# Kernel optimization log

Hardware: AMD Instinct MI355X
Metric: run time of the kernel (lower is better)

## Reference

```python
import jax, jax.numpy as jnp
import numpy as np
from jax import lax

BSZ, BEAM, VOCAB, D = 32, 4, 50257, 1024
MAXLEN = 64
L = MAXLEN + 2            # tokens buffer length (bos + maxlen+1 slots)
SLEN = MAXLEN + 1         # scores buffer length
PAD, EOS, UNK = 1, 2, 3
TEMP = 1.0
LEN_PEN = 1.0
UNK_PEN = 0.0
NEG = jnp.float32(-1e9)   # stand-in for -inf (safe for grads)


def setup_inputs() -> dict:
    key = jax.random.key(0)
    k1, k2, k3 = jax.random.split(key, 3)
    # 0.02 scaling keeps logits in a realistic range
    emb = jax.random.normal(k1, (VOCAB, D), jnp.float32) * 0.02
    W_out = jax.random.normal(k2, (D, VOCAB), jnp.float32) * 0.02
    pos_emb = jax.random.normal(k3, (SLEN, D), jnp.float32) * 0.02
    return {"emb": emb, "W_out": W_out, "pos_emb": pos_emb}


def _decode(emb, W_out, pos_emb, tokens, step):
    # stand-in decoder: prev-token embedding + pos embedding -> vocab logits
    prev = lax.dynamic_index_in_dim(tokens, step, axis=1, keepdims=False)  # [bbsz]
    h = emb[prev] + pos_emb[step]                                          # [bbsz, D]
    lp = jax.nn.log_softmax((h @ W_out) / TEMP, axis=-1)                   # [bbsz, V]
    lp = lp.at[:, PAD].set(NEG)
    lp = lp.at[:, UNK].add(-UNK_PEN)
    return lp


def _beam_search(emb, W_out, pos_emb):
    bbsz = BSZ * BEAM
    tokens = jnp.full((bbsz, L), PAD, jnp.int32).at[:, 0].set(EOS)
    scores = jnp.zeros((bbsz, SLEN), jnp.float32)
    fin_tok = jnp.zeros((BSZ, BEAM, L), jnp.int32)
    fin_sc = jnp.full((BSZ, BEAM), NEG, jnp.float32)
    offsets = jnp.arange(2 * BEAM, dtype=jnp.int32)
    colL = jnp.arange(L)
    colS = jnp.arange(SLEN)
    barange = jnp.arange(BEAM)

    def step_fn(carry, step):
        tokens, scores, fin_tok, fin_sc = carry
        lp = _decode(emb, W_out, pos_emb, tokens, step).reshape(BSZ, BEAM, VOCAB)
        prev_sc = lax.dynamic_index_in_dim(scores, jnp.maximum(step - 1, 0), axis=1, keepdims=False)
        prev_sc = jnp.where(step == 0, 0.0, prev_sc).reshape(BSZ, BEAM)
        cum = lp + prev_sc[:, :, None]
        # step 0: only the first beam participates (fairseq BeamSearch.step)
        cum = jnp.where((step == 0) & (barange[None, :, None] > 0), NEG, cum)
        cand_sc, cand_flat = lax.top_k(cum.reshape(BSZ, BEAM * VOCAB), 2 * BEAM)
        cand_beam = cand_flat // VOCAB       # [BSZ, 2*BEAM]
        cand_tok = cand_flat % VOCAB
        tokens3 = tokens.reshape(BSZ, BEAM, L)
        # --- finalize eos hypotheses from the first BEAM candidates ---
        eos_mask_b = cand_tok[:, :BEAM] == EOS
        eos_norm = jnp.where(eos_mask_b, cand_sc[:, :BEAM] / (step + 1.0) ** LEN_PEN, NEG)
        eos_tok = jnp.take_along_axis(tokens3, cand_beam[:, :BEAM, None], axis=1)
        eos_tok = jnp.where(colL[None, None, :] == step + 1, EOS, eos_tok)
        all_sc = jnp.concatenate([fin_sc, eos_norm], axis=1)
        all_tok = jnp.concatenate([fin_tok, eos_tok], axis=1)
        fin_sc, sel = lax.top_k(all_sc, BEAM)
        fin_tok = jnp.take_along_axis(all_tok, sel[:, :, None], axis=1)
        # --- pick BEAM active (non-eos) hypotheses (smallest active_mask) ---
        eos_mask = (cand_tok == EOS).astype(jnp.int32)
        amask = eos_mask * (2 * BEAM) + offsets[None, :]
        _, active = lax.top_k(-amask, BEAM)
        act_beam = jnp.take_along_axis(cand_beam, active, axis=1)
        act_tok = jnp.take_along_axis(cand_tok, active, axis=1)
        act_sc = jnp.take_along_axis(cand_sc, active, axis=1)
        # --- reorder beams, append new token / score ---
        tokens3 = jnp.take_along_axis(tokens3, act_beam[:, :, None], axis=1)
        tokens3 = jnp.where(colL[None, None, :] == step + 1, act_tok[:, :, None], tokens3)
        scores3 = jnp.take_along_axis(scores.reshape(BSZ, BEAM, SLEN), act_beam[:, :, None], axis=1)
        scores3 = jnp.where(colS[None, None, :] == step, act_sc[:, :, None], scores3)
        return (tokens3.reshape(bbsz, L), scores3.reshape(bbsz, SLEN), fin_tok, fin_sc), None

    carry = (tokens, scores, fin_tok, fin_sc)
    (tokens, scores, fin_tok, fin_sc), _ = lax.scan(step_fn, carry, jnp.arange(MAXLEN))
    # --- final step: force EOS on every surviving beam (step == maxlen) ---
    lp = _decode(emb, W_out, pos_emb, tokens, MAXLEN)
    eos_sc = (scores[:, MAXLEN - 1] + lp[:, EOS]).reshape(BSZ, BEAM) / (MAXLEN + 1.0) ** LEN_PEN
    tokens3 = tokens.reshape(BSZ, BEAM, L)
    eos_tok = jnp.where(jnp.arange(L)[None, None, :] == MAXLEN + 1, EOS, tokens3)
    all_sc = jnp.concatenate([fin_sc, eos_sc], axis=1)
    all_tok = jnp.concatenate([fin_tok, eos_tok], axis=1)
    fin_sc, sel = lax.top_k(all_sc, BEAM)
    fin_tok = jnp.take_along_axis(all_tok, sel[:, :, None], axis=1)
    return fin_tok, fin_sc


def reference(emb, W_out, pos_emb):
    # returns (finalized tokens [BSZ, BEAM, L] int32, normalized scores [BSZ, BEAM] f32)
    return _beam_search(emb, W_out, pos_emb)
```

## Files before the change

kernel.cpp:

```cpp
#include <hip/hip_runtime.h>
#include <cstdint>
#include <cstddef>

#define VOCAB_N 50257
#define NPAD    50304
#define DIM     1024
#define BSZ_N   32
#define BEAM_N  4
#define BB      128
#define L_N     66
#define SLEN_N  65
#define MAXLEN_N 64
#define PAD_T   1
#define EOS_T   2
#define NEGV    (-1e9f)
#define SENTV   (-3.402823466e38f)
#define PW_BLOCK 128

typedef unsigned long long u64;
typedef __attribute__((ext_vector_type(8))) _Float16 f16x8;
typedef __attribute__((ext_vector_type(4))) _Float16 f16x4;
typedef __attribute__((ext_vector_type(4))) float f32x4;

__device__ __constant__ int QLO[4] = {0, 12560, 25128, 37688};
__device__ __constant__ int QHI[4] = {12560, 25128, 37688, 50257};

struct PWTree {
    int nleaf, nint, maxlev, root;
    int lstart[256], lnum[256], lslot[256];
    int eL[256], eR[256], eD[256];
    int lvl[32];
};

constexpr PWTree build_tree(int start, int n0) {
    PWTree t{};
    int fs[64] = {}, fn[64] = {}, fstt[64] = {}, fls[64] = {}, fll[64] = {};
    int tL[256] = {}, tR[256] = {}, tD[256] = {}, tLev[256] = {};
    int sp = 0, lc = 0, nc = 0, cnt = 0;
    fs[0] = start; fn[0] = n0; fstt[0] = 0; sp = 1;
    int retslot = -1, retlev = 0;
    while (sp > 0) {
        const int n = fn[sp - 1], s = fs[sp - 1], st = fstt[sp - 1];
        if (n <= PW_BLOCK) {
            t.lstart[lc] = s; t.lnum[lc] = n; t.lslot[lc] = cnt;
            retslot = cnt; retlev = 0; ++cnt; ++lc; --sp; continue;
        }
        int L = (n >> 1); L -= (L & 7);
        if (st == 0)      { fstt[sp - 1] = 1; fs[sp] = s;     fn[sp] = L;     fstt[sp] = 0; ++sp; }
        else if (st == 1) { fls[sp - 1] = retslot; fll[sp - 1] = retlev; fstt[sp - 1] = 2;
                            fs[sp] = s + L; fn[sp] = n - L; fstt[sp] = 0; ++sp; }
        else {
            const int lv = (fll[sp - 1] > retlev ? fll[sp - 1] : retlev) + 1;
            tL[nc] = fls[sp - 1]; tR[nc] = retslot; tD[nc] = cnt; tLev[nc] = lv;
            retslot = cnt; retlev = lv; ++cnt; ++nc; --sp;
        }
    }
    int maxlev = 0;
    for (int j = 0; j < nc; ++j) if (tLev[j] > maxlev) maxlev = tLev[j];
    int cl[40] = {};
    for (int j = 0; j < nc; ++j) cl[tLev[j]]++;
    int acc = 0;
    for (int v = 1; v <= maxlev; ++v) { t.lvl[v] = acc; acc += cl[v]; }
    t.lvl[maxlev + 1] = acc;
    int pos[40] = {};
    for (int v = 1; v <= maxlev; ++v) pos[v] = t.lvl[v];
    for (int j = 0; j < nc; ++j) {
        const int v = tLev[j]; const int p = pos[v]++;
        t.eL[p] = tL[j]; t.eR[p] = tR[j]; t.eD[p] = tD[j];
    }
    t.nleaf = lc; t.nint = nc; t.maxlev = maxlev; t.root = retslot;
    return t;
}

__device__ constexpr PWTree g_q0 = build_tree(0, 12560);
__device__ constexpr PWTree g_q1 = build_tree(12560, 12568);
__device__ constexpr PWTree g_q2 = build_tree(25128, 12560);
__device__ constexpr PWTree g_q3 = build_tree(37688, 12569);

__device__ __forceinline__ unsigned sortable_f32(float x) {
    unsigned u = __float_as_uint(x);
    return (u & 0x80000000u) ? ~u : (u | 0x80000000u);
}
__device__ __forceinline__ float unsort_f32(unsigned s) {
    unsigned u = (s & 0x80000000u) ? (s & 0x7fffffffu) : ~s;
    return __uint_as_float(u);
}

__global__ void k_init(int* __restrict__ tokens, float* __restrict__ scores,
                       int* __restrict__ fin_tok, float* __restrict__ fin_sc,
                       unsigned* __restrict__ rmax_u) {
    int i = blockIdx.x * blockDim.x + threadIdx.x;
    int st = gridDim.x * blockDim.x;
    for (int k = i; k < BB * L_N; k += st) tokens[k] = ((k % L_N) == 0) ? EOS_T : PAD_T;
    for (int k = i; k < BB * SLEN_N; k += st) scores[k] = 0.f;
    for (int k = i; k < BB * L_N; k += st) fin_tok[k] = 0;
    for (int k = i; k < BB; k += st) { fin_sc[k] = NEGV; rmax_u[k] = 0u; }
}

__device__ __forceinline__ void split2(float x, _Float16& h0, _Float16& h1) {
    const float xs = x * 4096.f;
    h0 = (_Float16)xs;
    const float r = xs - (float)h0;
    h1 = (_Float16)r;
}


__global__ __launch_bounds__(256) void k_wsplit(const float* __restrict__ W,
                                                _Float16* __restrict__ Wsp) {
    const int bid = blockIdx.x;
    const int ct = bid % 786, kt = bid / 786;
    const int n0 = ct * 64, k0 = kt * 32;
    const int tid = threadIdx.x;
    const int c = tid & 63, kk4 = tid >> 6;
    _Float16 v0[8], v1[8];
#pragma unroll
    for (int j = 0; j < 8; ++j) {
        const int k = kk4 * 8 + j;
        float wv = 0.f;
        if (n0 + c < VOCAB_N) wv = W[(size_t)(k0 + k) * VOCAB_N + n0 + c];
        split2(wv, v0[j], v1[j]);
    }
    const size_t base0 = ((size_t)(kt * 2 + 0) * NPAD + n0 + c) * 32 + kk4 * 8;
    const size_t base1 = ((size_t)(kt * 2 + 1) * NPAD + n0 + c) * 32 + kk4 * 8;
    *(f16x8*)&Wsp[base0] = *(f16x8*)v0;
    *(f16x8*)&Wsp[base1] = *(f16x8*)v1;
}

__global__ __launch_bounds__(256) void k_hsplit(const float* __restrict__ emb,
                                                const float* __restrict__ pos_emb,
                                                const int* __restrict__ tokens,
                                                _Float16* __restrict__ Hsp, int step) {
    const int row = blockIdx.x;
    const int tid = threadIdx.x;
    const int tok = tokens[row * L_N + step];
    const int k4 = tid * 4;
    const int kt = k4 >> 5, kk = k4 & 31;
    const float4 e = *(const float4*)(emb + (size_t)tok * DIM + k4);
    const float4 p = *(const float4*)(pos_emb + (size_t)step * DIM + k4);
    const float hv[4] = {e.x + p.x, e.y + p.y, e.z + p.z, e.w + p.w};
    f16x4 o0, o1;
#pragma unroll
    for (int d = 0; d < 4; ++d) {
        _Float16 a0, a1;
        split2(hv[d], a0, a1);
        o0[d] = a0; o1[d] = a1;
    }
    *(f16x4*)&Hsp[((size_t)(kt * 2 + 0) * 128 + row) * 32 + kk] = o0;
    *(f16x4*)&Hsp[((size_t)(kt * 2 + 1) * 128 + row) * 32 + kk] = o1;
}

__global__ __launch_bounds__(512) void k_gemm_fast(const _Float16* __restrict__ Wsp,
                                                   const _Float16* __restrict__ Hsp,
                                                   float* __restrict__ logits,
                                                   unsigned* __restrict__ rmax_u) {
    __shared__ __align__(16) _Float16 Ha[2][128][40];
    __shared__ __align__(16) _Float16 Wb[2][128][40];
    __shared__ unsigned smax[128];
    const int tid = threadIdx.x;
    const int n0 = blockIdx.x * 128;
    const int lane = tid & 63, wid = tid >> 6;
    const int la = lane & 15, g = lane >> 4;
    const int wr = wid >> 1, wc = wid & 1;
    const int sidx = tid >> 2, sg = tid & 3;

    if (tid < 128) smax[tid] = 0u;

    f32x4 acc[2][4];
#pragma unroll
    for (int mf = 0; mf < 2; ++mf)
#pragma unroll
        for (int nf = 0; nf < 4; ++nf)
#pragma unroll
            for (int j = 0; j < 4; ++j) acc[mf][nf][j] = 0.f;

    const size_t WT = (size_t)2 * NPAD * 32;
    const size_t wbase = (size_t)n0 * 32 + tid * 8;
    const size_t hbase = (size_t)tid * 8;

    f16x8 rH0 = *(const f16x8*)&Hsp[hbase];
    f16x8 rH1 = *(const f16x8*)&Hsp[4096 + hbase];
    f16x8 rW0 = *(const f16x8*)&Wsp[wbase];
    f16x8 rW1 = *(const f16x8*)&Wsp[(size_t)NPAD * 32 + wbase];

    for (int t = 0; t < 32; ++t) {
        *(f16x8*)&Ha[0][sidx][sg * 8] = rH0;
        *(f16x8*)&Ha[1][sidx][sg * 8] = rH1;
        *(f16x8*)&Wb[0][sidx][sg * 8] = rW0;
        *(f16x8*)&Wb[1][sidx][sg * 8] = rW1;
        __syncthreads();
        if (t + 1 < 32) {
            const size_t ho = (size_t)(t + 1) * 8192;
            const size_t wo = (size_t)(t + 1) * WT;
            rH0 = *(const f16x8*)&Hsp[ho + hbase];
            rH1 = *(const f16x8*)&Hsp[ho + 4096 + hbase];
            rW0 = *(const f16x8*)&Wsp[wo + wbase];
            rW1 = *(const f16x8*)&Wsp[wo + (size_t)NPAD * 32 + wbase];
        }
        f16x8 a[2][2];
#pragma unroll
        for (int mf = 0; mf < 2; ++mf) {
            a[mf][0] = *(const f16x8*)&Ha[0][wr * 32 + mf * 16 + la][g * 8];
            a[mf][1] = *(const f16x8*)&Ha[1][wr * 32 + mf * 16 + la][g * 8];
        }
#pragma unroll
        for (int nf = 0; nf < 4; ++nf) {
            const int c = wc * 64 + nf * 16 + la;
            const f16x8 b0 = *(const f16x8*)&Wb[0][c][g * 8];
            const f16x8 b1 = *(const f16x8*)&Wb[1][c][g * 8];
#pragma unroll
            for (int mf = 0; mf < 2; ++mf) {
                f32x4 cc = acc[mf][nf];
                cc = __builtin_amdgcn_mfma_f32_16x16x32_f16(a[mf][0], b0, cc, 0, 0, 0);
                cc = __builtin_amdgcn_mfma_f32_16x16x32_f16(a[mf][0], b1, cc, 0, 0, 0);
                cc = __builtin_amdgcn_mfma_f32_16x16x32_f16(a[mf][1], b0, cc, 0, 0, 0);
                acc[mf][nf] = cc;
            }
        }
        __syncthreads();
    }

#pragma unroll
    for (int mf = 0; mf < 2; ++mf) {
        const int row = wr * 32 + mf * 16 + g * 4;
        float rmx[4] = {SENTV, SENTV, SENTV, SENTV};
#pragma unroll
        for (int nf = 0; nf < 4; ++nf) {
            const int col = n0 + wc * 64 + nf * 16 + la;
#pragma unroll
            for (int j = 0; j < 4; ++j) {
                const float v = acc[mf][nf][j] * 0x1p-24f;
                logits[(size_t)(row + j) * NPAD + col] = v;
                rmx[j] = fmaxf(rmx[j], v);
            }
        }
#pragma unroll
        for (int j = 0; j < 4; ++j) {
            float v = rmx[j];
            v = fmaxf(v, __shfl_xor(v, 1, 64));
            v = fmaxf(v, __shfl_xor(v, 2, 64));
            v = fmaxf(v, __shfl_xor(v, 4, 64));
            v = fmaxf(v, __shfl_xor(v, 8, 64));
            if (la == 0) atomicMax(&smax[row + j], sortable_f32(v));
        }
    }
    __syncthreads();
    if (tid < 128) atomicMax(&rmax_u[tid], smax[tid]);
}

#define KT 32
__global__ __launch_bounds__(512) void k_gemm_slow(const float* __restrict__ W,
                                                   const float* __restrict__ emb,
                                                   const float* __restrict__ pos_emb,
                                                   const int* __restrict__ tokens,
                                                   float* __restrict__ logits,
                                                   unsigned* __restrict__ rmax_u, int step) {
    __shared__ __align__(16) _Float16 Ha[2][128][40];
    __shared__ __align__(16) _Float16 Wb[2][128][40];
    __shared__ unsigned smax[128];
    const int tid = threadIdx.x;
    const int n0 = blockIdx.x * 128;
    const bool full = (n0 + 128 <= VOCAB_N);
    const int lane = tid & 63, wid = tid >> 6;
    const int wr = wid >> 1, wc = wid & 1;
    const int la = lane & 15, g = lane >> 4;
    const int hrow = tid & 127, hkq = tid >> 7;
    const int tokH = tokens[hrow * L_N + step];
    const float* eprow = emb + (size_t)tokH * DIM;
    const float* pprow = pos_emb + (size_t)step * DIM;
    const int wcq = tid & 31, wk = tid >> 5;

    if (tid < 128) smax[tid] = 0u;

    f32x4 acc[2][4];
#pragma unroll
    for (int mf = 0; mf < 2; ++mf)
#pragma unroll
        for (int nf = 0; nf < 4; ++nf)
#pragma unroll
            for (int j = 0; j < 4; ++j) acc[mf][nf][j] = 0.f;

    for (int k0 = 0; k0 < DIM; k0 += KT) {
#pragma unroll
        for (int d = 0; d < 4; ++d) {
            const int c = wcq + 32 * d;
#pragma unroll
            for (int qq = 0; qq < 2; ++qq) {
                const int kk = wk + 16 * qq;
                float wv = 0.f;
                if (full || (n0 + c < VOCAB_N))
                    wv = W[(size_t)(k0 + kk) * VOCAB_N + n0 + c];
                _Float16 b0, b1;
                split2(wv, b0, b1);
                Wb[0][c][kk] = b0;
                Wb[1][c][kk] = b1;
            }
        }
#pragma unroll
        for (int qq = 0; qq < 2; ++qq) {
            const int kq = hkq + 4 * qq;
            const float4 e0 = *(const float4*)(eprow + k0 + kq * 4);
            const float4 p0 = *(const float4*)(pprow + k0 + kq * 4);
            const float hv[4] = {e0.x + p0.x, e0.y + p0.y, e0.z + p0.z, e0.w + p0.w};
            f16x4 o0, o1;
#pragma unroll
            for (int d = 0; d < 4; ++d) {
                _Float16 a0, a1;
                split2(hv[d], a0, a1);
                o0[d] = a0; o1[d] = a1;
            }
            *(f16x4*)&Ha[0][hrow][kq * 4] = o0;
            *(f16x4*)&Ha[1][hrow][kq * 4] = o1;
        }
        __syncthreads();
        f16x8 af[2][2];
#pragma unroll
        for (int mf = 0; mf < 2; ++mf)
#pragma unroll
            for (int p = 0; p < 2; ++p)
                af[mf][p] = *(const f16x8*)&Ha[p][wr * 32 + mf * 16 + la][g * 8];
#pragma unroll
        for (int nf = 0; nf < 4; ++nf) {
            const int c = wc * 64 + nf * 16 + la;
            const f16x8 b0 = *(const f16x8*)&Wb[0][c][g * 8];
            const f16x8 b1 = *(const f16x8*)&Wb[1][c][g * 8];
#pragma unroll
            for (int mf = 0; mf < 2; ++mf) {
                f32x4 cc = acc[mf][nf];
                cc = __builtin_amdgcn_mfma_f32_16x16x32_f16(af[mf][0], b0, cc, 0, 0, 0);
                cc = __builtin_amdgcn_mfma_f32_16x16x32_f16(af[mf][0], b1, cc, 0, 0, 0);
                cc = __builtin_amdgcn_mfma_f32_16x16x32_f16(af[mf][1], b0, cc, 0, 0, 0);
                acc[mf][nf] = cc;
            }
        }
        __syncthreads();
    }
#pragma unroll
    for (int mf = 0; mf < 2; ++mf) {
        const int row = wr * 32 + mf * 16 + g * 4;
        float rmx[4] = {SENTV, SENTV, SENTV, SENTV};
#pragma unroll
        for (int nf = 0; nf < 4; ++nf) {
            const int col = n0 + wc * 64 + nf * 16 + la;
#pragma unroll
            for (int j = 0; j < 4; ++j) {
                const float v = acc[mf][nf][j] * 0x1p-24f;
                logits[(size_t)(row + j) * NPAD + col] = v;
                rmx[j] = fmaxf(rmx[j], v);
            }
        }
#pragma unroll
        for (int j = 0; j < 4; ++j) {
            float v = rmx[j];
            v = fmaxf(v, __shfl_xor(v, 1, 64));
            v = fmaxf(v, __shfl_xor(v, 2, 64));
            v = fmaxf(v, __shfl_xor(v, 4, 64));
            v = fmaxf(v, __shfl_xor(v, 8, 64));
            if (la == 0) atomicMax(&smax[row + j], sortable_f32(v));
        }
    }
    __syncthreads();
    if (tid < 128) atomicMax(&rmax_u[tid], smax[tid]);
}

__device__ __forceinline__ u64 pack_key(float x, int tk) {
    return ((u64)sortable_f32(x) << 32) | (unsigned)(VOCAB_N - tk);
}
__device__ __forceinline__ void insk16(u64 k, u64 lst[16]) {
#pragma unroll
    for (int p = 0; p < 16; ++p) {
        if (k > lst[p]) { u64 o = lst[p]; lst[p] = k; k = o; }
    }
}
__device__ __forceinline__ u64 wave_max_u64(u64 v) {
#pragma unroll
    for (int o = 32; o > 0; o >>= 1) {
        u64 w = __shfl_xor(v, o, 64);
        if (w > v) v = w;
    }
    return v;
}

#define RT2 256
__global__ __launch_bounds__(RT2) void k_scanexp(const float* __restrict__ logits,
                                                 const unsigned* __restrict__ rmax_u,
                                                 u64* __restrict__ htop,
                                                 float* __restrict__ qsum) {
    const int hb = blockIdx.x;
    const int row = hb >> 2, q = hb & 3;
    const int tid = threadIdx.x;
    const int lane = tid & 63, wid = tid >> 6;
    const float* x = logits + (size_t)row * NPAD;
    const int lo = QLO[q], hi = QHI[q];
    const float mrow = unsort_f32(rmax_u[row]);

    u64 lst[16];
#pragma unroll
    for (int p = 0; p < 16; ++p) lst[p] = 0ULL;
    for (int v = lo + tid * 4; v + 3 < hi; v += RT2 * 4) {
        const float4 t = *(const float4*)(x + v);
        const float va[4] = {t.x, t.y, t.z, t.w};
#pragma unroll
        for (int u = 0; u < 4; ++u) {
            const int tk = v + u;
            if (tk == PAD_T) continue;
            const u64 key = pack_key(va[u], tk);
            if (key > lst[15]) insk16(key, lst);
        }
    }
    if (q == 3 && tid == 0) {
        const int tk = VOCAB_N - 1;
        const u64 key = pack_key(x[tk], tk);
        if (key > lst[15]) insk16(key, lst);
    }

    __shared__ u64 wtop[4][16];
    for (int pass = 0; pass < 16; ++pass) {
        const u64 cand = lst[0];
        const u64 mx = wave_max_u64(cand);
        const u64 ball = __ballot(cand == mx);
        const int first = __ffsll((u64)ball) - 1;
        if (lane == first) {
#pragma unroll
            for (int p = 0; p < 15; ++p) lst[p] = lst[p + 1];
            lst[15] = 0ULL;
        }
        if (lane == 0) wtop[wid][pass] = mx;
    }
    __syncthreads();

    __shared__ u64 sfin[16];
    if (tid < 64) {
        const u64 mine = wtop[tid >> 4][tid & 15];
        bool taken = false;
        for (int pass = 0; pass < 16; ++pass) {
            const u64 cand = taken ? 0ULL : mine;
            const u64 mx = wave_max_u64(cand);
            const u64 ball = __ballot(cand == mx);
            const int first = __ffsll((u64)ball) - 1;
            if (tid == first) taken = true;
            if (tid == 0) sfin[pass] = mx;
        }
    }

    const PWTree& T = (q == 0) ? g_q0 : (q == 1) ? g_q1 : (q == 2) ? g_q2 : g_q3;
    __shared__ float slot[512];
    for (int leaf = tid; leaf < T.nleaf; leaf += RT2) {
        const int s = T.lstart[leaf];
        const int n = T.lnum[leaf];
        float res;
        if (n < 8) {
            res = 0.f;
            for (int i = 0; i < n; ++i) res += expf(x[s + i] - mrow);
        } else {
            float r0 = expf(x[s + 0] - mrow), r1 = expf(x[s + 1] - mrow);
            float r2 = expf(x[s + 2] - mrow), r3 = expf(x[s + 3] - mrow);
            float r4 = expf(x[s + 4] - mrow), r5 = expf(x[s + 5] - mrow);
            float r6 = expf(x[s + 6] - mrow), r7 = expf(x[s + 7] - mrow);
            int i = 8;
            const int lim = n - (n & 7);
            for (; i < lim; i += 8) {
                r0 += expf(x[s + i + 0] - mrow); r1 += expf(x[s + i + 1] - mrow);
                r2 += expf(x[s + i + 2] - mrow); r3 += expf(x[s + i + 3] - mrow);
                r4 += expf(x[s + i + 4] - mrow); r5 += expf(x[s + i + 5] - mrow);
                r6 += expf(x[s + i + 6] - mrow); r7 += expf(x[s + i + 7] - mrow);
            }
            res = ((r0 + r1) + (r2 + r3)) + ((r4 + r5) + (r6 + r7));
            for (; i < n; ++i) res += expf(x[s + i] - mrow);
        }
        slot[T.lslot[leaf]] = res;
    }
    __syncthreads();
    for (int lev = 1; lev <= T.maxlev; ++lev) {
        for (int j = T.lvl[lev] + tid; j < T.lvl[lev + 1]; j += RT2)
            slot[T.eD[j]] = slot[T.eL[j]] + slot[T.eR[j]];
        __syncthreads();
    }
    if (tid == 0) qsum[hb] = slot[T.root];
    if (tid < 16) htop[hb * 16 + tid] = sfin[tid];
}

__global__ __launch_bounds__(256) void k_beam(const u64* __restrict__ htop,
                                              unsigned* __restrict__ rmax_u,
                                              const float* __restrict__ qsum,
                                              int* __restrict__ tokens,
                                              float* __restrict__ scores,
                                              int* __restrict__ fin_tok,
                                              float* __restrict__ fin_sc,
                                              const float* __restrict__ emb,
                                              const float* __restrict__ pos_emb,
                                              _Float16* __restrict__ Hsp,
                                              int step) {
    const int sent = blockIdx.x;
    const int tid = threadIdx.x;
    const int rN = (step == 0) ? 1 : BEAM_N;

    __shared__ u64 keys[4][64];
    for (int e = tid; e < 256; e += 256) {
        const int r = e >> 6, i = e & 63;
        keys[r][i] = htop[((sent * BEAM_N + r) * 4 + (i >> 4)) * 16 + (i & 15)];
    }
    __syncthreads();

    __shared__ u64 merged[4][16];
    if (tid < 4) {
        int ia[4] = {0, 0, 0, 0};
        for (int o = 0; o < 16; ++o) {
            u64 best = 0ULL; int bq = 0;
#pragma unroll
            for (int qq = 0; qq < 4; ++qq) {
                const u64 h = (ia[qq] < 16) ? keys[tid][qq * 16 + ia[qq]] : 0ULL;
                if (h > best) { best = h; bq = qq; }
            }
            merged[tid][o] = best; ia[bq]++;
        }
    }
    __syncthreads();

    __shared__ float bval[64]; __shared__ int bflat[64];
    if (tid < 16 * rN) {
        const int r = tid >> 4, j = tid & 15;
        const int row = sent * BEAM_N + r;
        const float rm = unsort_f32(rmax_u[row]);
        const float rl = (float)log((double)((qsum[row * 4] + qsum[row * 4 + 1]) +
                                             (qsum[row * 4 + 2] + qsum[row * 4 + 3])));
        const float prev = (step == 0) ? 0.f : scores[row * SLEN_N + step - 1];
        const u64 k = merged[r][j];
        const float xv = unsort_f32((unsigned)(k >> 32));
        const int   tk = VOCAB_N - (int)(k & 0xFFFFFFFFu);
        bval[tid]  = ((xv - rm) - rl) + prev;
        bflat[tid] = r * VOCAB_N + tk;
    }
    __syncthreads();
    __shared__ float cand_sc[8]; __shared__ int cand_flat[8];
    if (tid == 0) {
        const int nC = 16 * rN;
        for (int pass = 0; pass < 8; ++pass) {
            float bv = SENTV; int bi = 0x7fffffff; int bs = -1;
            for (int k = 0; k < nC; ++k) {
                const float v = bval[k]; const int ix = bflat[k];
                if (v > bv || (v == bv && ix < bi)) { bv = v; bi = ix; bs = k; }
            }
            cand_sc[pass] = bv; cand_flat[pass] = bi;
            bval[bs] = SENTV; bflat[bs] = 0x7fffffff;
        }
    }
    __syncthreads();

    __shared__ int   cur_tok[BEAM_N * L_N];
    __shared__ int   cur_fin[BEAM_N * L_N];
    __shared__ float cur_sc[BEAM_N * SLEN_N];
    for (int e = tid; e < BEAM_N * L_N; e += 256) {
        cur_tok[e] = tokens[sent * (BEAM_N * L_N) + e];
        cur_fin[e] = fin_tok[sent * (BEAM_N * L_N) + e];
    }
    for (int e = tid; e < BEAM_N * SLEN_N; e += 256)
        cur_sc[e] = scores[sent * (BEAM_N * SLEN_N) + e];
    __syncthreads();

    __shared__ int   tmp_fin[BEAM_N * L_N];
    __shared__ int   tmp_tok[BEAM_N * L_N];
    __shared__ float tmp_sc[BEAM_N * SLEN_N];
    __shared__ float nfin_s[BEAM_N];
    if (tid == 0) {
        int cb[8], ct[8];
#pragma unroll
        for (int j = 0; j < 8; ++j) {
            cb[j] = cand_flat[j] / VOCAB_N;
            ct[j] = cand_flat[j] % VOCAB_N;
        }
        float allsc[8];
#pragma unroll
        for (int j = 0; j < 4; ++j) allsc[j] = fin_sc[sent * BEAM_N + j];
#pragma unroll
        for (int j = 0; j < 4; ++j)
            allsc[4 + j] = (ct[j] == EOS_T) ? (cand_sc[j] / (float)(step + 1)) : NEGV;
        int fsel[4]; float nfin[4];
        bool used[8] = {false,false,false,false,false,false,false,false};
#pragma unroll
        for (int b = 0; b < 4; ++b) {
            int best = -1; float bvv = 0.f;
#pragma unroll
            for (int j = 0; j < 8; ++j) {
                if (used[j]) continue;
                if (best < 0 || allsc[j] > bvv) { best = j; bvv = allsc[j]; }
            }
            used[best] = true; fsel[b] = best; nfin[b] = bvv;
        }
#pragma unroll
        for (int b = 0; b < 4; ++b) {
            const int s = fsel[b];
            if (s < 4) {
                for (int p = 0; p < L_N; ++p) tmp_fin[b * L_N + p] = cur_fin[s * L_N + p];
            } else {
                const int bm = cb[s - 4];
                for (int p = 0; p < L_N; ++p)
                    tmp_fin[b * L_N + p] = (p == step + 1) ? EOS_T : cur_tok[bm * L_N + p];
            }
        }
        int ab[4], atk[4]; float asc[4]; int na = 0;
#pragma unroll
        for (int j = 0; j < 8; ++j) {
            if (na < 4 && ct[j] != EOS_T) { ab[na] = cb[j]; atk[na] = ct[j]; asc[na] = cand_sc[j]; ++na; }
        }
#pragma unroll
        for (int b = 0; b < 4; ++b) {
            const int bm = ab[b];
            for (int p = 0; p < L_N; ++p)
                tmp_tok[b * L_N + p] = (p == step + 1) ? atk[b] : cur_tok[bm * L_N + p];
            for (int p = 0; p < SLEN_N; ++p)
                tmp_sc[b * SLEN_N + p] = (p == step) ? asc[b] : cur_sc[bm * SLEN_N + p];
        }
#pragma unroll
        for (int b = 0; b < 4; ++b) nfin_s[b] = nfin[b];
    }
    __syncthreads();

    for (int e = tid; e < BEAM_N * L_N; e += 256) {
        fin_tok[sent * (BEAM_N * L_N) + e] = tmp_fin[e];
        tokens[sent * (BEAM_N * L_N) + e]  = tmp_tok[e];
    }
    for (int e = tid; e < BEAM_N * SLEN_N; e += 256)
        scores[sent * (BEAM_N * SLEN_N) + e] = tmp_sc[e];
    if (tid < 4) {
        fin_sc[sent * BEAM_N + tid] = nfin_s[tid];
        rmax_u[sent * BEAM_N + tid] = 0u;
    }

    {
        const int nstep = step + 1;
        const int r = tid >> 6;
        const int row = sent * BEAM_N + r;
        const int tok = tmp_tok[r * L_N + nstep];
        const int kb = (tid & 63) * 16;
        const int kt = kb >> 5, kk0 = kb & 31;
        const float* ep = emb + (size_t)tok * DIM + kb;
        const float* pp = pos_emb + (size_t)nstep * DIM + kb;
        _Float16 v0[16], v1[16];
#pragma unroll
        for (int jj = 0; jj < 4; ++jj) {
            const float4 e = *(const float4*)(ep + jj * 4);
            const float4 p = *(const float4*)(pp + jj * 4);
            const float hv[4] = {e.x + p.x, e.y + p.y, e.z + p.z, e.w + p.w};
#pragma unroll
            for (int d = 0; d < 4; ++d)
                split2(hv[d], v0[jj * 4 + d], v1[jj * 4 + d]);
        }
        _Float16* d0 = &Hsp[((size_t)(kt * 2 + 0) * 128 + row) * 32 + kk0];
        _Float16* d1 = &Hsp[((size_t)(kt * 2 + 1) * 128 + row) * 32 + kk0];
        *(f16x8*)d0       = *(f16x8*)&v0[0];
        *(f16x8*)(d0 + 8) = *(f16x8*)&v0[8];
        *(f16x8*)d1       = *(f16x8*)&v1[0];
        *(f16x8*)(d1 + 8) = *(f16x8*)&v1[8];
    }
}

__global__ __launch_bounds__(256) void k_final(const float* __restrict__ logits,
                                               const unsigned* __restrict__ rmax_u,
                                               const float* __restrict__ qsum,
                                               const int* __restrict__ tokens,
                                               const float* __restrict__ scores,
                                               const int* __restrict__ fin_tok,
                                               const float* __restrict__ fin_sc,
                                               float* __restrict__ out) {
    const int sent = blockIdx.x;
    const int tid = threadIdx.x;
    __shared__ int fsel_s[4]; __shared__ float nfin_s[4];
    if (tid == 0) {
        float allsc[8];
#pragma unroll
        for (int r = 0; r < 4; ++r) {
            const int row = sent * BEAM_N + r;
            const float rm = unsort_f32(rmax_u[row]);
            const float rl = (float)log((double)((qsum[row * 4] + qsum[row * 4 + 1]) +
                                                 (qsum[row * 4 + 2] + qsum[row * 4 + 3])));
            const float lpE = ((logits[(size_t)row * NPAD + EOS_T] - rm) - rl);
            allsc[r] = fin_sc[sent * BEAM_N + r];
            allsc[4 + r] = (scores[row * SLEN_N + (MAXLEN_N - 1)] + lpE) / 65.0f;
        }
        bool used[8] = {false,false,false,false,false,false,false,false};
#pragma unroll
        for (int b = 0; b < 4; ++b) {
            int best = -1; float bvv = 0.f;
#pragma unroll
            for (int j = 0; j < 8; ++j) {
                if (used[j]) continue;
                if (best < 0 || allsc[j] > bvv) { best = j; bvv = allsc[j]; }
            }
            used[best] = true; fsel_s[b] = best; nfin_s[b] = bvv;
        }
    }
    __syncthreads();
    for (int e = tid; e < BEAM_N * L_N; e += 256) {
        const int b = e / L_N, p = e % L_N;
        const int s = fsel_s[b]; int valt;
        if (s < 4) {
            valt = fin_tok[(sent * BEAM_N + s) * L_N + p];
        } else {
            const int r = s - 4;
            valt = (p == MAXLEN_N + 1) ? EOS_T : tokens[(sent * BEAM_N + r) * L_N + p];
        }
        out[(size_t)(sent * BEAM_N + b) * L_N + p] = (float)valt;
    }
    if (tid < 4) out[BSZ_N * BEAM_N * L_N + sent * BEAM_N + tid] = nfin_s[tid];
}

extern "C" void kernel_launch(void* const* d_in, const int* in_sizes, int n_in,
                              void* d_out, int out_size, void* d_ws, size_t ws_size,
                              hipStream_t stream) {
    const float* emb = (const float*)d_in[0];
    const float* W   = (const float*)d_in[1];
    const float* pos = (const float*)d_in[2];
    float* out = (float*)d_out;

    char* w = (char*)d_ws;
    size_t off = 0;
    auto alloc = [&](size_t bytes) { void* p = w + off; off += (bytes + 15) & ~(size_t)15; return p; };
    float*    logits = (float*)alloc((size_t)BB * NPAD * 4);
    unsigned* rmax_u = (unsigned*)alloc(BB * 4);
    float*    qsum   = (float*)alloc(BB * 4 * 4);
    u64*      htop   = (u64*)alloc((size_t)BB * 4 * 16 * 8);
    int*      tokens = (int*)alloc(BB * L_N * 4);
    float*    scores = (float*)alloc(BB * SLEN_N * 4);
    int*      ftok   = (int*)alloc(BB * L_N * 4);
    float*    fsc    = (float*)alloc(BB * 4);
    _Float16* Wsp    = (_Float16*)alloc((size_t)2 * NPAD * 1024 * 2);
    _Float16* Hsp    = (_Float16*)alloc((size_t)2 * 128 * 1024 * 2);
    const bool fast = (off <= ws_size);

    k_init<<<32, 256, 0, stream>>>(tokens, scores, ftok, fsc, rmax_u);
    if (fast) {
        k_wsplit<<<786 * 32, 256, 0, stream>>>(W, Wsp);
        k_hsplit<<<128, 256, 0, stream>>>(emb, pos, tokens, Hsp, 0);
    }
    for (int s = 0; s < MAXLEN_N; ++s) {
        if (fast) {
            k_gemm_fast<<<NPAD / 128, 512, 0, stream>>>(Wsp, Hsp, logits, rmax_u);
        } else {
            k_gemm_slow<<<NPAD / 128, 512, 0, stream>>>(W, emb, pos, tokens, logits, rmax_u, s);
        }
        k_scanexp<<<BB * 4, RT2, 0, stream>>>(logits, rmax_u, htop, qsum);
        k_beam<<<BSZ_N, 256, 0, stream>>>(htop, rmax_u, qsum, tokens, scores, ftok, fsc,
                                          emb, pos, Hsp, s);
    }
    if (fast) {
        k_gemm_fast<<<NPAD / 128, 512, 0, stream>>>(Wsp, Hsp, logits, rmax_u);
    } else {
        k_gemm_slow<<<NPAD / 128, 512, 0, stream>>>(W, emb, pos, tokens, logits, rmax_u, MAXLEN_N);
    }
    k_scanexp<<<BB * 4, RT2, 0, stream>>>(logits, rmax_u, htop, qsum);
    k_final<<<BSZ_N, 256, 0, stream>>>(logits, rmax_u, qsum, tokens, scores, ftok, fsc, out);
}
```

Measured before the change: 11.35 ms.

## Double-buffer LDS in fast GEMM and halve N-tile to 64 columns

The fast GEMM kernel now uses 64-column tiles with 256 threads, giving twice as many blocks (786) to spread across CUs. It also adds double-buffered shared memory with two register prefetch sets, so global loads and LDS stores for the next K-tiles overlap the MFMA work on the current tile. This removes one barrier-bound stall per K step. The cost is more total H traffic, since each block reloads the full 128-row H, plus more register pressure from the extra prefetch set.

After: 12.16 ms. 7.1% more time.

```diff
diff --git a/kernel.cpp b/kernel.cpp
--- a/kernel.cpp
+++ b/kernel.cpp
@@ -149,19 +149,62 @@
     *(f16x4*)&Hsp[((size_t)(kt * 2 + 1) * 128 + row) * 32 + kk] = o1;
 }
 
-__global__ __launch_bounds__(512) void k_gemm_fast(const _Float16* __restrict__ Wsp,
+#define LOADSET(S, t)                                                         \
+    S##h0a = *(const f16x8*)&Hsp[(size_t)(t) * 8192 + tid * 16];              \
+    S##h0b = *(const f16x8*)&Hsp[(size_t)(t) * 8192 + tid * 16 + 8];          \
+    S##h1a = *(const f16x8*)&Hsp[(size_t)(t) * 8192 + 4096 + tid * 16];       \
+    S##h1b = *(const f16x8*)&Hsp[(size_t)(t) * 8192 + 4096 + tid * 16 + 8];   \
+    S##w0  = *(const f16x8*)&Wsp[(size_t)(t) * WT + wbase];                   \
+    S##w1  = *(const f16x8*)&Wsp[(size_t)(t) * WT + WPL + wbase];
+
+#define STORESET(S, buf)                                                      \
+    *(f16x8*)&Ha[buf][0][hR][hK]     = S##h0a;                                \
+    *(f16x8*)&Ha[buf][0][hR][hK + 8] = S##h0b;                                \
+    *(f16x8*)&Ha[buf][1][hR][hK]     = S##h1a;                                \
+    *(f16x8*)&Ha[buf][1][hR][hK + 8] = S##h1b;                                \
+    *(f16x8*)&Wb[buf][0][wR][wK]     = S##w0;                                 \
+    *(f16x8*)&Wb[buf][1][wR][wK]     = S##w1;
+
+#define COMPUTE(buf)                                                          \
+    {                                                                         \
+        f16x8 a00 = *(const f16x8*)&Ha[buf][0][wr * 32 + la][g * 8];          \
+        f16x8 a01 = *(const f16x8*)&Ha[buf][1][wr * 32 + la][g * 8];          \
+        f16x8 a10 = *(const f16x8*)&Ha[buf][0][wr * 32 + 16 + la][g * 8];     \
+        f16x8 a11 = *(const f16x8*)&Ha[buf][1][wr * 32 + 16 + la][g * 8];     \
+        _Pragma("unroll")                                                     \
+        for (int nf = 0; nf < 4; ++nf) {                                      \
+            const f16x8 b0 = *(const f16x8*)&Wb[buf][0][nf * 16 + la][g * 8]; \
+            const f16x8 b1 = *(const f16x8*)&Wb[buf][1][nf * 16 + la][g * 8]; \
+            f32x4 c0 = acc[0][nf];                                            \
+            c0 = __builtin_amdgcn_mfma_f32_16x16x32_f16(a00, b0, c0, 0, 0, 0);\
+            c0 = __builtin_amdgcn_mfma_f32_16x16x32_f16(a00, b1, c0, 0, 0, 0);\
+            c0 = __builtin_amdgcn_mfma_f32_16x16x32_f16(a01, b0, c0, 0, 0, 0);\
+            acc[0][nf] = c0;                                                  \
+            f32x4 c1 = acc[1][nf];                                            \
+            c1 = __builtin_amdgcn_mfma_f32_16x16x32_f16(a10, b0, c1, 0, 0, 0);\
+            c1 = __builtin_amdgcn_mfma_f32_16x16x32_f16(a10, b1, c1, 0, 0, 0);\
+            c1 = __builtin_amdgcn_mfma_f32_16x16x32_f16(a11, b0, c1, 0, 0, 0);\
+            acc[1][nf] = c1;                                                  \
+        }                                                                     \
+    }
+
+__global__ __launch_bounds__(256) void k_gemm_fast(const _Float16* __restrict__ Wsp,
                                                    const _Float16* __restrict__ Hsp,
                                                    float* __restrict__ logits,
                                                    unsigned* __restrict__ rmax_u) {
-    __shared__ __align__(16) _Float16 Ha[2][128][40];
-    __shared__ __align__(16) _Float16 Wb[2][128][40];
+    __shared__ __align__(16) _Float16 Ha[2][2][128][40];
+    __shared__ __align__(16) _Float16 Wb[2][2][64][40];
     __shared__ unsigned smax[128];
     const int tid = threadIdx.x;
-    const int n0 = blockIdx.x * 128;
-    const int lane = tid & 63, wid = tid >> 6;
+    const int n0 = blockIdx.x * 64;
+    const int lane = tid & 63;
+    const int wr = tid >> 6;
     const int la = lane & 15, g = lane >> 4;
-    const int wr = wid >> 1, wc = wid & 1;
-    const int sidx = tid >> 2, sg = tid & 3;
+    const int hR = tid >> 1, hK = (tid & 1) * 16;
+    const int wR = tid >> 2, wK = (tid & 3) * 8;
+    const size_t WT  = (size_t)2 * NPAD * 32;
+    const size_t WPL = (size_t)NPAD * 32;
+    const size_t wbase = (size_t)n0 * 32 + tid * 8;
 
     if (tid < 128) smax[tid] = 0u;
 
@@ -173,49 +216,23 @@
 #pragma unroll
             for (int j = 0; j < 4; ++j) acc[mf][nf][j] = 0.f;
 
-    const size_t WT = (size_t)2 * NPAD * 32;
-    const size_t wbase = (size_t)n0 * 32 + tid * 8;
-    const size_t hbase = (size_t)tid * 8;
-
-    f16x8 rH0 = *(const f16x8*)&Hsp[hbase];
-    f16x8 rH1 = *(const f16x8*)&Hsp[4096 + hbase];
-    f16x8 rW0 = *(const f16x8*)&Wsp[wbase];
-    f16x8 rW1 = *(const f16x8*)&Wsp[(size_t)NPAD * 32 + wbase];
-
-    for (int t = 0; t < 32; ++t) {
-        *(f16x8*)&Ha[0][sidx][sg * 8] = rH0;
-        *(f16x8*)&Ha[1][sidx][sg * 8] = rH1;
-        *(f16x8*)&Wb[0][sidx][sg * 8] = rW0;
-        *(f16x8*)&Wb[1][sidx][sg * 8] = rW1;
+    f16x8 Ah0a, Ah0b, Ah1a, Ah1b, Aw0, Aw1;
+    f16x8 Bh0a, Bh0b, Bh1a, Bh1b, Bw0, Bw1;
+
+    LOADSET(A, 0)
+    LOADSET(B, 1)
+    STORESET(A, 0)
+    __syncthreads();
+
+    for (int tt = 0; tt < 16; ++tt) {
+        const int t0 = 2 * tt;
+        if (t0 + 2 < 32) { LOADSET(A, t0 + 2) }
+        STORESET(B, 1)
+        COMPUTE(0)
         __syncthreads();
-        if (t + 1 < 32) {
-            const size_t ho = (size_t)(t + 1) * 8192;
-            const size_t wo = (size_t)(t + 1) * WT;
-            rH0 = *(const f16x8*)&Hsp[ho + hbase];
-            rH1 = *(const f16x8*)&Hsp[ho + 4096 + hbase];
-            rW0 = *(const f16x8*)&Wsp[wo + wbase];
-            rW1 = *(const f16x8*)&Wsp[wo + (size_t)NPAD * 32 + wbase];
-        }
-        f16x8 a[2][2];
-#pragma unroll
-        for (int mf = 0; mf < 2; ++mf) {
-            a[mf][0] = *(const f16x8*)&Ha[0][wr * 32 + mf * 16 + la][g * 8];
-            a[mf][1] = *(const f16x8*)&Ha[1][wr * 32 + mf * 16 + la][g * 8];
-        }
-#pragma unroll
-        for (int nf = 0; nf < 4; ++nf) {
-            const int c = wc * 64 + nf * 16 + la;
-            const f16x8 b0 = *(const f16x8*)&Wb[0][c][g * 8];
-            const f16x8 b1 = *(const f16x8*)&Wb[1][c][g * 8];
-#pragma unroll
-            for (int mf = 0; mf < 2; ++mf) {
-                f32x4 cc = acc[mf][nf];
-                cc = __builtin_amdgcn_mfma_f32_16x16x32_f16(a[mf][0], b0, cc, 0, 0, 0);
-                cc = __builtin_amdgcn_mfma_f32_16x16x32_f16(a[mf][0], b1, cc, 0, 0, 0);
-                cc = __builtin_amdgcn_mfma_f32_16x16x32_f16(a[mf][1], b0, cc, 0, 0, 0);
-                acc[mf][nf] = cc;
-            }
-        }
+        if (t0 + 3 < 32) { LOADSET(B, t0 + 3) }
+        if (t0 + 2 < 32) { STORESET(A, 0) }
+        COMPUTE(1)
         __syncthreads();
     }
 
@@ -225,7 +242,7 @@
         float rmx[4] = {SENTV, SENTV, SENTV, SENTV};
 #pragma unroll
         for (int nf = 0; nf < 4; ++nf) {
-            const int col = n0 + wc * 64 + nf * 16 + la;
+            const int col = n0 + nf * 16 + la;
 #pragma unroll
             for (int j = 0; j < 4; ++j) {
                 const float v = acc[mf][nf][j] * 0x1p-24f;
@@ -254,8 +271,8 @@
                                                    const int* __restrict__ tokens,
                                                    float* __restrict__ logits,
                                                    unsigned* __restrict__ rmax_u, int step) {
-    __shared__ __align__(16) _Float16 Ha[2][128][40];
-    __shared__ __align__(16) _Float16 Wb[2][128][40];
+    __shared__ __align__(16) _Float16 Has[2][128][40];
+    __shared__ __align__(16) _Float16 Wbs[2][128][40];
     __shared__ unsigned smax[128];
     const int tid = threadIdx.x;
     const int n0 = blockIdx.x * 128;
@@ -291,8 +308,8 @@
                     wv = W[(size_t)(k0 + kk) * VOCAB_N + n0 + c];
                 _Float16 b0, b1;
                 split2(wv, b0, b1);
-                Wb[0][c][kk] = b0;
-                Wb[1][c][kk] = b1;
+                Wbs[0][c][kk] = b0;
+                Wbs[1][c][kk] = b1;
             }
         }
 #pragma unroll
@@ -308,8 +325,8 @@
                 split2(hv[d], a0, a1);
                 o0[d] = a0; o1[d] = a1;
             }
-            *(f16x4*)&Ha[0][hrow][kq * 4] = o0;
-            *(f16x4*)&Ha[1][hrow][kq * 4] = o1;
+            *(f16x4*)&Has[0][hrow][kq * 4] = o0;
+            *(f16x4*)&Has[1][hrow][kq * 4] = o1;
         }
         __syncthreads();
         f16x8 af[2][2];
@@ -317,12 +334,12 @@
         for (int mf = 0; mf < 2; ++mf)
 #pragma unroll
             for (int p = 0; p < 2; ++p)
-                af[mf][p] = *(const f16x8*)&Ha[p][wr * 32 + mf * 16 + la][g * 8];
+                af[mf][p] = *(const f16x8*)&Has[p][wr * 32 + mf * 16 + la][g * 8];
 #pragma unroll
         for (int nf = 0; nf < 4; ++nf) {
             const int c = wc * 64 + nf * 16 + la;
-            const f16x8 b0 = *(const f16x8*)&Wb[0][c][g * 8];
-            const f16x8 b1 = *(const f16x8*)&Wb[1][c][g * 8];
+            const f16x8 b0 = *(const f16x8*)&Wbs[0][c][g * 8];
+            const f16x8 b1 = *(const f16x8*)&Wbs[1][c][g * 8];
 #pragma unroll
             for (int mf = 0; mf < 2; ++mf) {
                 f32x4 cc = acc[mf][nf];
@@ -734,7 +751,7 @@
     }
     for (int s = 0; s < MAXLEN_N; ++s) {
         if (fast) {
-            k_gemm_fast<<<NPAD / 128, 512, 0, stream>>>(Wsp, Hsp, logits, rmax_u);
+            k_gemm_fast<<<NPAD / 64, 256, 0, stream>>>(Wsp, Hsp, logits, rmax_u);
         } else {
             k_gemm_slow<<<NPAD / 128, 512, 0, stream>>>(W, emb, pos, tokens, logits, rmax_u, s);
         }
@@ -743,7 +760,7 @@
                                           emb, pos, Hsp, s);
     }
     if (fast) {
-        k_gemm_fast<<<NPAD / 128, 512, 0, stream>>>(Wsp, Hsp, logits, rmax_u);
+        k_gemm_fast<<<NPAD / 64, 256, 0, stream>>>(Wsp, Hsp, logits, rmax_u);
     } else {
         k_gemm_slow<<<NPAD / 128, 512, 0, stream>>>(W, emb, pos, tokens, logits, rmax_u, MAXLEN_N);
     }
```
